# Kernel tuning notes

Hardware: AMD Instinct MI355X
Metric: run time of the kernel (lower is better)

The kernel has to match this reference:

```python
import jax, jax.numpy as jnp
import numpy as np

D_IN = 200
H = 1024
OUT = 1095
L = 12
B = 128
T = 20


def setup_inputs() -> dict:
    key = jax.random.key(0)
    ks = jax.random.split(key, 10)
    s = lambda k, shape, fan: (jax.random.normal(k, shape, jnp.float32) / np.sqrt(fan)).astype(jnp.float32)
    return {
        "x": jax.random.normal(ks[0], (B, T, D_IN), jnp.float32),
        "hidden": jnp.zeros((L, B, H), jnp.float32),
        "W1": s(ks[1], (D_IN, H), D_IN),
        "b1": jnp.zeros((H,), jnp.float32),
        # SRU per-layer weights: input -> [x_tilde, f_gate, r_gate] (3H), plus biases for f,r (2H)
        "sru_W": s(ks[2], (L, H, 3 * H), H),
        "sru_b": jnp.zeros((L, 2 * H), jnp.float32),
        "W3": s(ks[3], (H, 1024), H),
        "b3": jnp.zeros((1024,), jnp.float32),
        "W4": s(ks[4], (1024, OUT), 1024),
        "b4": jnp.zeros((OUT,), jnp.float32),
    }


def _sru_layer(x_tbh, c0, W_l, b_l):
    # x_tbh: [T,B,H]; c0: [B,H]
    U = jnp.einsum("tbh,hk->tbk", x_tbh, W_l)  # [T,B,3H]
    x_tilde, f_pre, r_pre = jnp.split(U, 3, axis=-1)
    b_f, b_r = jnp.split(b_l, 2)
    f = jax.nn.sigmoid(f_pre + b_f)
    r = jax.nn.sigmoid(r_pre + b_r)

    def step(c, inp):
        xt, ft, rt, x_in = inp
        c = ft * c + (1.0 - ft) * xt
        h = rt * jnp.tanh(c) + (1.0 - rt) * x_in  # highway (use_tanh=True)
        return c, h

    c_T, h_seq = jax.lax.scan(step, c0, (x_tilde, f, r, x_tbh))
    return h_seq, c_T


def reference(x, hidden, W1, b1, sru_W, sru_b, W3, b3, W4, b4):
    b, t, _ = x.shape
    # Dense_layer1 (dropout is identity in eval)
    h = x.reshape(b * t, -1) @ W1 + b1
    h = h.reshape(b, t, H).transpose(1, 0, 2)  # [T,B,H]
    cs = []
    for l in range(L):
        h, c_T = _sru_layer(h, hidden[l], sru_W[l], sru_b[l])
        cs.append(c_T)
    hidden_after = jnp.stack(cs, axis=0)  # [L,B,H]
    h = h.transpose(1, 0, 2).reshape(b * t, H)
    fx = h @ W3 + b3
    y = jax.nn.relu(fx)
    logits = (y @ W4 + b4).reshape(-1, OUT)
    return logits, fx, hidden_after
```

## Files before the change

### kernel.cpp

```cpp
#include <hip/hip_runtime.h>

#define D_IN  200
#define KPAD1 224
#define HDIM  1024
#define OUTN  1095
#define NPAD4 1152
#define LNUM  12
#define BB    128
#define TT    20
#define MROWS (BB * TT)

typedef __bf16 bf16;
typedef __attribute__((ext_vector_type(8))) __bf16 bf16x8;
typedef __attribute__((ext_vector_type(4))) float floatx4;

__device__ __forceinline__ bool res_f32(int dt, int inf32) {
  return dt == 1 || (dt == 2 && inf32 != 0);
}

__global__ __launch_bounds__(64) void detect_k(const unsigned int* __restrict__ w,
                                               int* __restrict__ flag) {
  int cnt = 0;
  for (int i = threadIdx.x; i < 1024; i += 64) {
    unsigned int ex = (w[i] >> 7) & 0xFFu;
    if (ex >= 104u && ex <= 131u) cnt++;
  }
  #pragma unroll
  for (int off = 32; off; off >>= 1) cnt += __shfl_down(cnt, off);
  if (threadIdx.x == 0) *flag = (cnt > 512) ? 0 : 1;
}

__global__ __launch_bounds__(256) void transp_k(
    const void* __restrict__ in, const int* __restrict__ dflag,
    bf16* __restrict__ out, int K, int N, int Kpad, int Npad,
    unsigned long long in_bs, unsigned long long out_bs)
{
  __shared__ float tile[32][33];
  const int inf32 = *dflag;
  const int tx = threadIdx.x & 31, ty = threadIdx.x >> 5;
  const int kt = blockIdx.x * 32, nt = blockIdx.y * 32;
  const float* inf = (const float*)in + (size_t)blockIdx.z * in_bs;
  const bf16*  inb = (const bf16*)in + (size_t)blockIdx.z * in_bs;
  #pragma unroll
  for (int j = 0; j < 4; j++) {
    const int k = kt + ty + j * 8, n = nt + tx;
    float v = 0.f;
    if (k < K && n < N)
      v = inf32 ? inf[(size_t)k * N + n] : (float)inb[(size_t)k * N + n];
    tile[ty + j * 8][tx] = v;
  }
  __syncthreads();
  bf16* o = out + (size_t)blockIdx.z * out_bs;
  #pragma unroll
  for (int j = 0; j < 4; j++) {
    const int n = nt + ty + j * 8, k = kt + tx;
    if (n < Npad && k < Kpad) o[(size_t)n * Kpad + k] = (bf16)tile[tx][ty + j * 8];
  }
}

__global__ __launch_bounds__(256) void convx_k(
    const void* __restrict__ x, const int* __restrict__ dflag, bf16* __restrict__ xc)
{
  const int inf32 = *dflag;
  const int idx = blockIdx.x * 256 + threadIdx.x;
  if (idx >= MROWS * KPAD1) return;
  const int row = idx / KPAD1;
  const int d = idx - row * KPAD1;
  const int t = row / BB, b = row - t * BB;
  float v = 0.f;
  if (d < D_IN) {
    const size_t src = ((size_t)b * TT + t) * D_IN + d;
    v = inf32 ? ((const float*)x)[src] : (float)((const bf16*)x)[src];
  }
  xc[idx] = (bf16)v;
}

__global__ __launch_bounds__(256) void gemm_f(
    const bf16* __restrict__ A, const bf16* __restrict__ Bt,
    const void* __restrict__ bias, unsigned long long bias_eoff,
    const int* __restrict__ dflag,
    void* __restrict__ out0, unsigned long long out0_eoff, int o0_dt,
    bf16* __restrict__ out1,
    int N, int Ks, int remapP, int remapQ)
{
  __shared__ bf16 As[128 * 32];
  __shared__ bf16 Bs[128 * 32];
  const int inf32 = *dflag;
  const bool o0f = res_f32(o0_dt, inf32);

  const int tid = threadIdx.x;
  const int wave = tid >> 6, lane = tid & 63;
  const int wr = wave >> 1, wc = wave & 1;
  const int lm = lane & 15, q = lane >> 4;
  const int l4r = lane >> 2, l4k = (lane & 3) * 8;

  const int bm = blockIdx.x * 128, bn = blockIdx.y * 128;

  int ar0 = bm + wave * 32 + l4r;
  int ar1 = ar0 + 16;
  if (remapP) {
    ar0 = (ar0 % remapP) * remapQ + ar0 / remapP;
    ar1 = (ar1 % remapP) * remapQ + ar1 / remapP;
  }
  const bf16* gA0 = A + (size_t)ar0 * Ks + l4k;
  const bf16* gA1 = A + (size_t)ar1 * Ks + l4k;
  const bf16* gB0 = Bt + (size_t)(bn + wave * 32 + l4r) * Ks + l4k;
  const bf16* gB1 = gB0 + (size_t)16 * Ks;

  auto* As3 = (__attribute__((address_space(3))) char*)As;
  auto* Bs3 = (__attribute__((address_space(3))) char*)Bs;
  const int lds0 = (wave * 32) * 64;
  const int lds1 = lds0 + 16 * 64;

  floatx4 acc[4][4];
  #pragma unroll
  for (int i = 0; i < 4; i++)
    #pragma unroll
    for (int j = 0; j < 4; j++) acc[i][j] = (floatx4){0.f, 0.f, 0.f, 0.f};

  for (int k0 = 0; k0 < Ks; k0 += 32) {
    __builtin_amdgcn_global_load_lds((const __attribute__((address_space(1))) void*)gA0,
                                     (__attribute__((address_space(3))) void*)(As3 + lds0), 16, 0, 0);
    __builtin_amdgcn_global_load_lds((const __attribute__((address_space(1))) void*)gA1,
                                     (__attribute__((address_space(3))) void*)(As3 + lds1), 16, 0, 0);
    __builtin_amdgcn_global_load_lds((const __attribute__((address_space(1))) void*)gB0,
                                     (__attribute__((address_space(3))) void*)(Bs3 + lds0), 16, 0, 0);
    __builtin_amdgcn_global_load_lds((const __attribute__((address_space(1))) void*)gB1,
                                     (__attribute__((address_space(3))) void*)(Bs3 + lds1), 16, 0, 0);
    gA0 += 32; gA1 += 32; gB0 += 32; gB1 += 32;
    __syncthreads();

    bf16x8 af[4], bfr[4];
    #pragma unroll
    for (int mi = 0; mi < 4; mi++)
      af[mi] = *(const bf16x8*)&As[(wr * 64 + mi * 16 + lm) * 32 + q * 8];
    #pragma unroll
    for (int ni = 0; ni < 4; ni++)
      bfr[ni] = *(const bf16x8*)&Bs[(wc * 64 + ni * 16 + lm) * 32 + q * 8];
    #pragma unroll
    for (int mi = 0; mi < 4; mi++)
      #pragma unroll
      for (int ni = 0; ni < 4; ni++)
        acc[mi][ni] = __builtin_amdgcn_mfma_f32_16x16x32_bf16(af[mi], bfr[ni], acc[mi][ni], 0, 0, 0);
    __syncthreads();
  }

  const int row_base = bm + wr * 64 + q * 4;
  const int col_base = bn + wc * 64 + lm;
  #pragma unroll
  for (int ni = 0; ni < 4; ni++) {
    const int c = col_base + ni * 16;
    if (c >= N) continue;
    float bv = 0.f;
    if (bias)
      bv = inf32 ? ((const float*)bias)[bias_eoff + c]
                 : (float)((const bf16*)bias)[bias_eoff + c];
    #pragma unroll
    for (int mi = 0; mi < 4; mi++)
      #pragma unroll
      for (int reg = 0; reg < 4; reg++) {
        const int r = row_base + mi * 16 + reg;
        const float v = acc[mi][ni][reg] + bv;
        const size_t o = (size_t)r * N + c;
        if (o0f) ((float*)out0)[out0_eoff + o] = v;
        else     ((bf16*)out0)[out0_eoff + o] = (bf16)v;
        if (out1) out1[o] = (bf16)(v > 0.f ? v : 0.f);
      }
  }
}

#define BM 64
#define BN 64
#define BK 32
#define LDSP (BK + 8)

__global__ __launch_bounds__(256) void gemm_k(
    const void* __restrict__ A, const void* __restrict__ Bm,
    const void* __restrict__ bias,
    void* __restrict__ out0, unsigned long long out0_eoff, int o0_dt,
    bf16* __restrict__ out1,
    const int* __restrict__ dflag,
    unsigned long long b_eoff, unsigned long long bias_eoff,
    int M, int N, int K, int remapP, int remapQ, int a_dt)
{
  __shared__ bf16 As[BM][LDSP];
  __shared__ bf16 Bs[BN][LDSP];

  const int inf32 = *dflag;
  const bool af32 = res_f32(a_dt, inf32);
  const bool bf32 = (inf32 != 0);
  const bool o0f  = res_f32(o0_dt, inf32);

  const int tid = threadIdx.x;
  const int bm = blockIdx.x * BM;
  const int bn = blockIdx.y * BN;

  const int a_r = tid >> 2;
  const int a_k = (tid & 3) * 8;
  int a_row = bm + a_r;
  const bool a_ok = a_row < M;
  if (remapP) a_row = (a_row % remapP) * remapQ + (a_row / remapP);
  const size_t a_off = (size_t)a_row * (size_t)K;

  const int b_k = tid >> 3;
  const int b_ng = bn + (tid & 7) * 8;
  const int b_nl = (tid & 7) * 8;
  const bool n_vec = ((N & 7) == 0) && (b_ng + 8 <= N);

  const int wave = tid >> 6;
  const int lane = tid & 63;
  const int wm = (wave >> 1) * 32;
  const int wn = (wave & 1) * 32;
  const int lm = lane & 15;
  const int q  = lane >> 4;

  floatx4 acc00 = {0.f,0.f,0.f,0.f}, acc01 = {0.f,0.f,0.f,0.f};
  floatx4 acc10 = {0.f,0.f,0.f,0.f}, acc11 = {0.f,0.f,0.f,0.f};

  for (int k0 = 0; k0 < K; k0 += BK) {
    {
      union { bf16x8 v; bf16 e[8]; } av;
      const int kg = k0 + a_k;
      if (af32) {
        const float* Af = (const float*)A;
        if (a_ok && (kg + 8 <= K)) {
          floatx4 f0 = *(const floatx4*)(Af + a_off + kg);
          floatx4 f1 = *(const floatx4*)(Af + a_off + kg + 4);
          #pragma unroll
          for (int e = 0; e < 4; e++) { av.e[e] = (bf16)f0[e]; av.e[4 + e] = (bf16)f1[e]; }
        } else {
          #pragma unroll
          for (int e = 0; e < 8; e++) {
            const int kk = kg + e;
            av.e[e] = (a_ok && kk < K) ? (bf16)Af[a_off + kk] : (bf16)0.f;
          }
        }
      } else {
        const bf16* Ab = (const bf16*)A;
        if (a_ok && (kg + 8 <= K)) {
          av.v = *(const bf16x8*)(Ab + a_off + kg);
        } else {
          #pragma unroll
          for (int e = 0; e < 8; e++) {
            const int kk = kg + e;
            av.e[e] = (a_ok && kk < K) ? Ab[a_off + kk] : (bf16)0.f;
          }
        }
      }
      *(bf16x8*)&As[a_r][a_k] = av.v;
    }
    {
      union { bf16x8 v; bf16 e[8]; } bv;
      const int kg = k0 + b_k;
      if (bf32) {
        const float* Bf = (const float*)Bm + b_eoff;
        if ((kg < K) && n_vec) {
          floatx4 f0 = *(const floatx4*)(Bf + (size_t)kg * N + b_ng);
          floatx4 f1 = *(const floatx4*)(Bf + (size_t)kg * N + b_ng + 4);
          #pragma unroll
          for (int e = 0; e < 4; e++) { bv.e[e] = (bf16)f0[e]; bv.e[4 + e] = (bf16)f1[e]; }
        } else {
          #pragma unroll
          for (int e = 0; e < 8; e++) {
            const int nn = b_ng + e;
            bv.e[e] = (kg < K && nn < N) ? (bf16)Bf[(size_t)kg * N + nn] : (bf16)0.f;
          }
        }
      } else {
        const bf16* Bb = (const bf16*)Bm + b_eoff;
        if ((kg < K) && n_vec) {
          bv.v = *(const bf16x8*)(Bb + (size_t)kg * N + b_ng);
        } else {
          #pragma unroll
          for (int e = 0; e < 8; e++) {
            const int nn = b_ng + e;
            bv.e[e] = (kg < K && nn < N) ? Bb[(size_t)kg * N + nn] : (bf16)0.f;
          }
        }
      }
      #pragma unroll
      for (int e = 0; e < 8; e++) Bs[b_nl + e][b_k] = bv.e[e];
    }
    __syncthreads();

    const bf16x8 a0 = *(const bf16x8*)&As[wm + lm][q * 8];
    const bf16x8 a1 = *(const bf16x8*)&As[wm + 16 + lm][q * 8];
    const bf16x8 b0 = *(const bf16x8*)&Bs[wn + lm][q * 8];
    const bf16x8 b1 = *(const bf16x8*)&Bs[wn + 16 + lm][q * 8];
    acc00 = __builtin_amdgcn_mfma_f32_16x16x32_bf16(a0, b0, acc00, 0, 0, 0);
    acc01 = __builtin_amdgcn_mfma_f32_16x16x32_bf16(a0, b1, acc01, 0, 0, 0);
    acc10 = __builtin_amdgcn_mfma_f32_16x16x32_bf16(a1, b0, acc10, 0, 0, 0);
    acc11 = __builtin_amdgcn_mfma_f32_16x16x32_bf16(a1, b1, acc11, 0, 0, 0);
    __syncthreads();
  }

  floatx4 accs[2][2] = {{acc00, acc01}, {acc10, acc11}};
  const int r0 = bm + wm + q * 4;
  const int c0 = bn + wn + lm;
  #pragma unroll
  for (int i = 0; i < 2; i++) {
    #pragma unroll
    for (int j = 0; j < 2; j++) {
      const int c = c0 + j * 16;
      if (c >= N) continue;
      float bias_v = 0.f;
      if (bias) {
        bias_v = inf32 ? ((const float*)bias)[bias_eoff + c]
                       : (float)((const bf16*)bias)[bias_eoff + c];
      }
      #pragma unroll
      for (int reg = 0; reg < 4; reg++) {
        const int r = r0 + i * 16 + reg;
        if (r >= M) continue;
        const float v = accs[i][j][reg] + bias_v;
        const size_t o = (size_t)r * (size_t)N + c;
        if (o0f) ((float*)out0)[out0_eoff + o] = v;
        else     ((bf16*)out0)[out0_eoff + o] = (bf16)v;
        if (out1) out1[o] = (bf16)(v > 0.f ? v : 0.f);
      }
    }
  }
}

__device__ __forceinline__ float sigmoidf_(float x) { return 1.f / (1.f + __expf(-x)); }
__device__ __forceinline__ float tanhf_(float x)    { return 1.f - 2.f / (__expf(2.f * x) + 1.f); }

__global__ __launch_bounds__(256) void sru_scan_k(
    const void* __restrict__ U, int u_f32,
    bf16* __restrict__ h,
    const void* __restrict__ c0, unsigned long long c0_eoff,
    const void* __restrict__ bvec, unsigned long long bvec_eoff,
    const int* __restrict__ dflag,
    void* __restrict__ cout, unsigned long long cout_eoff)
{
  const int inf32 = *dflag;
  const int idx = blockIdx.x * 256 + threadIdx.x;
  const int hh = idx & (HDIM - 1);
  const int b = idx >> 10;
  const float bf_ = inf32 ? ((const float*)bvec)[bvec_eoff + hh]
                          : (float)((const bf16*)bvec)[bvec_eoff + hh];
  const float br_ = inf32 ? ((const float*)bvec)[bvec_eoff + HDIM + hh]
                          : (float)((const bf16*)bvec)[bvec_eoff + HDIM + hh];
  float c = inf32 ? ((const float*)c0)[c0_eoff + idx]
                  : (float)((const bf16*)c0)[c0_eoff + idx];
  const float* Uf = (const float*)U;
  const bf16*  Ub = (const bf16*)U;
  #pragma unroll 4
  for (int t = 0; t < TT; t++) {
    const size_t off = (size_t)(t * BB + b) * (size_t)(3 * HDIM);
    const float xt = u_f32 ? Uf[off + hh] : (float)Ub[off + hh];
    const float fp = u_f32 ? Uf[off + HDIM + hh] : (float)Ub[off + HDIM + hh];
    const float rp = u_f32 ? Uf[off + 2 * HDIM + hh] : (float)Ub[off + 2 * HDIM + hh];
    const float fg = sigmoidf_(fp + bf_);
    const float rg = sigmoidf_(rp + br_);
    c = fg * c + (1.f - fg) * xt;
    const size_t hi = (size_t)t * (BB * HDIM) + idx;
    const float xin = (float)h[hi];
    h[hi] = (bf16)(rg * tanhf_(c) + (1.f - rg) * xin);
  }
  if (inf32) ((float*)cout)[cout_eoff + idx] = c;
  else       ((bf16*)cout)[cout_eoff + idx] = (bf16)c;
}

extern "C" void kernel_launch(void* const* d_in, const int* in_sizes, int n_in,
                              void* d_out, int out_size, void* d_ws, size_t ws_size,
                              hipStream_t stream) {
  const void* x       = d_in[0];
  const void* hidden0 = d_in[1];
  const void* W1      = d_in[2];
  const void* b1      = d_in[3];
  const void* sru_W   = d_in[4];
  const void* sru_b   = d_in[5];
  const void* W3      = d_in[6];
  const void* b3      = d_in[7];
  const void* W4      = d_in[8];
  const void* b4      = d_in[9];

  const unsigned long long eo_fx  = (unsigned long long)MROWS * OUTN;
  const unsigned long long eo_hid = eo_fx + (unsigned long long)MROWS * HDIM;

  const size_t z_flag = 256;
  const size_t z_hA   = (size_t)MROWS * HDIM * 2;
  const size_t z_U    = (size_t)MROWS * 3 * HDIM * 4;
  const size_t z_xc   = (size_t)MROWS * KPAD1 * 2;
  const size_t z_W1T  = (size_t)HDIM * KPAD1 * 2;
  const size_t z_sWT  = (size_t)LNUM * 3 * HDIM * HDIM * 2;
  const size_t z_W3T  = (size_t)HDIM * HDIM * 2;
  const size_t z_W4T  = (size_t)NPAD4 * HDIM * 2;
  const size_t FAST_NEED = z_flag + z_hA + z_U + z_xc + z_W1T + z_sWT + z_W3T + z_W4T;

  int* dflag = (int*)d_ws;
  char* p = (char*)d_ws + z_flag;
  bf16*  hA    = (bf16*)p;            p += z_hA;
  char*  Ubase = p;                   p += z_U;
  bf16*  xc    = (bf16*)p;            p += z_xc;
  bf16*  W1T   = (bf16*)p;            p += z_W1T;
  bf16*  sWT   = (bf16*)p;            p += z_sWT;
  bf16*  W3T   = (bf16*)p;            p += z_W3T;
  bf16*  W4T   = (bf16*)p;
  void*  U = (void*)Ubase;
  bf16*  y = (bf16*)Ubase;

  dim3 blk(256);
  detect_k<<<1, 64, 0, stream>>>((const unsigned int*)W1, dflag);

  if (ws_size >= FAST_NEED) {
    convx_k<<<dim3((MROWS * KPAD1 + 255) / 256), blk, 0, stream>>>(x, dflag, xc);
    transp_k<<<dim3(KPAD1 / 32, HDIM / 32, 1), blk, 0, stream>>>(
        W1, dflag, W1T, D_IN, HDIM, KPAD1, HDIM, 0ull, 0ull);
    transp_k<<<dim3(HDIM / 32, 3 * HDIM / 32, LNUM), blk, 0, stream>>>(
        sru_W, dflag, sWT, HDIM, 3 * HDIM, HDIM, 3 * HDIM,
        (unsigned long long)HDIM * 3 * HDIM, (unsigned long long)3 * HDIM * HDIM);
    transp_k<<<dim3(HDIM / 32, HDIM / 32, 1), blk, 0, stream>>>(
        W3, dflag, W3T, HDIM, HDIM, HDIM, HDIM, 0ull, 0ull);
    transp_k<<<dim3(HDIM / 32, NPAD4 / 32, 1), blk, 0, stream>>>(
        W4, dflag, W4T, HDIM, OUTN, HDIM, NPAD4, 0ull, 0ull);

    gemm_f<<<dim3(MROWS / 128, HDIM / 128), blk, 0, stream>>>(
        xc, W1T, b1, 0ull, dflag, hA, 0ull, 0, nullptr, HDIM, KPAD1, 0, 0);

    for (int l = 0; l < LNUM; l++) {
      gemm_f<<<dim3(MROWS / 128, 3 * HDIM / 128), blk, 0, stream>>>(
          hA, sWT + (size_t)l * 3 * HDIM * HDIM, nullptr, 0ull, dflag,
          U, 0ull, 1, nullptr, 3 * HDIM, HDIM, 0, 0);
      sru_scan_k<<<dim3((BB * HDIM) / 256), blk, 0, stream>>>(
          U, 1, hA, hidden0, (unsigned long long)l * BB * HDIM,
          sru_b, (unsigned long long)l * 2 * HDIM,
          dflag, d_out, eo_hid + (unsigned long long)l * BB * HDIM);
    }

    gemm_f<<<dim3(MROWS / 128, HDIM / 128), blk, 0, stream>>>(
        hA, W3T, b3, 0ull, dflag, d_out, eo_fx, 2, y, HDIM, HDIM, TT, BB);

    gemm_f<<<dim3(MROWS / 128, NPAD4 / 128), blk, 0, stream>>>(
        y, W4T, b4, 0ull, dflag, d_out, 0ull, 2, nullptr, OUTN, HDIM, 0, 0);
  } else {
    const size_t need_f32U = z_flag + z_hA + z_U;
    const int u_f32 = (ws_size >= need_f32U) ? 1 : 0;

    gemm_k<<<dim3(MROWS / BM, HDIM / BN), blk, 0, stream>>>(
        x, W1, b1, hA, 0ull, 0, nullptr, dflag, 0ull, 0ull,
        MROWS, HDIM, D_IN, BB, TT, 2);

    for (int l = 0; l < LNUM; l++) {
      gemm_k<<<dim3(MROWS / BM, (3 * HDIM) / BN), blk, 0, stream>>>(
          hA, sru_W, nullptr, U, 0ull, (u_f32 ? 1 : 0), nullptr, dflag,
          (unsigned long long)l * HDIM * 3 * HDIM, 0ull,
          MROWS, 3 * HDIM, HDIM, 0, 0, 0);
      sru_scan_k<<<dim3((BB * HDIM) / 256), blk, 0, stream>>>(
          U, u_f32, hA, hidden0, (unsigned long long)l * BB * HDIM,
          sru_b, (unsigned long long)l * 2 * HDIM,
          dflag, d_out, eo_hid + (unsigned long long)l * BB * HDIM);
    }

    gemm_k<<<dim3(MROWS / BM, HDIM / BN), blk, 0, stream>>>(
        hA, W3, b3, d_out, eo_fx, 2, y, dflag, 0ull, 0ull,
        MROWS, HDIM, HDIM, TT, BB, 0);

    gemm_k<<<dim3(MROWS / BM, (OUTN + BN - 1) / BN), blk, 0, stream>>>(
        y, W4, b4, d_out, 0ull, 2, nullptr, dflag, 0ull, 0ull,
        MROWS, OUTN, HDIM, 0, 0, 0);
  }
}
```

Measured before the change: 931.2 us.

## Store SRU gate buffer in bf16, vectorize scan, and widen weight transposes

The SRU projection GEMM now writes U as bf16 instead of fp32, which halves the write and read traffic between the GEMM and the scan. A new scan kernel processes two hidden units per thread with paired bf16 loads and stores. The large weight transposes switch to a 64x64-tile kernel that uses float4 reads and 16-byte bf16 writes. The cost is extra rounding of the gate pre-activations to bf16 before the sigmoid and the recurrence.

```diff
diff --git a/kernel.cpp b/kernel.cpp
--- a/kernel.cpp
+++ b/kernel.cpp
@@ -11,7 +11,9 @@
 #define MROWS (BB * TT)
 
 typedef __bf16 bf16;
+typedef __attribute__((ext_vector_type(2))) __bf16 bf16x2;
 typedef __attribute__((ext_vector_type(8))) __bf16 bf16x8;
+typedef __attribute__((ext_vector_type(2))) float floatx2;
 typedef __attribute__((ext_vector_type(4))) float floatx4;
 
 __device__ __forceinline__ bool res_f32(int dt, int inf32) {
@@ -28,6 +30,51 @@
   #pragma unroll
   for (int off = 32; off; off >>= 1) cnt += __shfl_down(cnt, off);
   if (threadIdx.x == 0) *flag = (cnt > 512) ? 0 : 1;
+}
+
+__global__ __launch_bounds__(256) void ftransp_k(
+    const void* __restrict__ in, const int* __restrict__ dflag,
+    bf16* __restrict__ out, int K, int N, int Npad,
+    unsigned long long in_bs, unsigned long long out_bs)
+{
+  __shared__ float tile[64][69];
+  const int inf32 = *dflag;
+  const int t = threadIdx.x;
+  const int kt = blockIdx.x * 64, nt = blockIdx.y * 64;
+  const float* inf = (const float*)in + (size_t)blockIdx.z * in_bs;
+  const bf16*  inb = (const bf16*)in + (size_t)blockIdx.z * in_bs;
+
+  const int lk = t >> 2;
+  const size_t rbase = (size_t)(kt + lk) * N;
+  #pragma unroll
+  for (int j = 0; j < 4; j++) {
+    const int ln = ((t & 3) + 4 * j) * 4;
+    const int gn = nt + ln;
+    floatx4 v = {0.f, 0.f, 0.f, 0.f};
+    if (inf32) {
+      if (gn + 4 <= N) {
+        v = *(const floatx4*)(inf + rbase + gn);
+      } else {
+        #pragma unroll
+        for (int e = 0; e < 4; e++) if (gn + e < N) v[e] = inf[rbase + gn + e];
+      }
+    } else {
+      #pragma unroll
+      for (int e = 0; e < 4; e++) if (gn + e < N) v[e] = (float)inb[rbase + gn + e];
+    }
+    #pragma unroll
+    for (int e = 0; e < 4; e++) tile[lk][ln + e] = v[e];
+  }
+  __syncthreads();
+
+  const int n  = t >> 2;
+  const int kc = (t & 3) * 16;
+  union { bf16x8 v[2]; bf16 e[16]; } o;
+  #pragma unroll
+  for (int i = 0; i < 16; i++) o.e[i] = (bf16)tile[kc + i][n];
+  bf16* op = out + (size_t)blockIdx.z * out_bs + (size_t)(nt + n) * K + kt + kc;
+  *(bf16x8*)op = o.v[0];
+  *(bf16x8*)(op + 8) = o.v[1];
 }
 
 __global__ __launch_bounds__(256) void transp_k(
@@ -325,6 +372,55 @@
 __device__ __forceinline__ float sigmoidf_(float x) { return 1.f / (1.f + __expf(-x)); }
 __device__ __forceinline__ float tanhf_(float x)    { return 1.f - 2.f / (__expf(2.f * x) + 1.f); }
 
+__global__ __launch_bounds__(256) void sru_scan2_k(
+    const bf16* __restrict__ U,
+    bf16* __restrict__ h,
+    const void* __restrict__ c0, unsigned long long c0_eoff,
+    const void* __restrict__ bvec, unsigned long long bvec_eoff,
+    const int* __restrict__ dflag,
+    void* __restrict__ cout, unsigned long long cout_eoff)
+{
+  const int inf32 = *dflag;
+  const int i2 = (blockIdx.x * 256 + threadIdx.x) * 2;
+  const int hh = i2 & (HDIM - 1);
+  const int b = i2 >> 10;
+  float bf_[2], br_[2], c[2];
+  #pragma unroll
+  for (int e = 0; e < 2; e++) {
+    bf_[e] = inf32 ? ((const float*)bvec)[bvec_eoff + hh + e]
+                   : (float)((const bf16*)bvec)[bvec_eoff + hh + e];
+    br_[e] = inf32 ? ((const float*)bvec)[bvec_eoff + HDIM + hh + e]
+                   : (float)((const bf16*)bvec)[bvec_eoff + HDIM + hh + e];
+    c[e] = inf32 ? ((const float*)c0)[c0_eoff + i2 + e]
+                 : (float)((const bf16*)c0)[c0_eoff + i2 + e];
+  }
+  #pragma unroll 4
+  for (int t = 0; t < TT; t++) {
+    const size_t off = (size_t)(t * BB + b) * (size_t)(3 * HDIM);
+    const bf16x2 xt2 = *(const bf16x2*)(U + off + hh);
+    const bf16x2 fp2 = *(const bf16x2*)(U + off + HDIM + hh);
+    const bf16x2 rp2 = *(const bf16x2*)(U + off + 2 * HDIM + hh);
+    const size_t hi = (size_t)t * (BB * HDIM) + i2;
+    const bf16x2 hin2 = *(const bf16x2*)(h + hi);
+    bf16x2 ho;
+    #pragma unroll
+    for (int e = 0; e < 2; e++) {
+      const float fg = sigmoidf_((float)fp2[e] + bf_[e]);
+      const float rg = sigmoidf_((float)rp2[e] + br_[e]);
+      c[e] = fg * c[e] + (1.f - fg) * (float)xt2[e];
+      ho[e] = (bf16)(rg * tanhf_(c[e]) + (1.f - rg) * (float)hin2[e]);
+    }
+    *(bf16x2*)(h + hi) = ho;
+  }
+  if (inf32) {
+    floatx2 co; co[0] = c[0]; co[1] = c[1];
+    *(floatx2*)((float*)cout + cout_eoff + i2) = co;
+  } else {
+    bf16x2 co; co[0] = (bf16)c[0]; co[1] = (bf16)c[1];
+    *(bf16x2*)((bf16*)cout + cout_eoff + i2) = co;
+  }
+}
+
 __global__ __launch_bounds__(256) void sru_scan_k(
     const void* __restrict__ U, int u_f32,
     bf16* __restrict__ h,
@@ -398,8 +494,8 @@
   bf16*  sWT   = (bf16*)p;            p += z_sWT;
   bf16*  W3T   = (bf16*)p;            p += z_W3T;
   bf16*  W4T   = (bf16*)p;
-  void*  U = (void*)Ubase;
-  bf16*  y = (bf16*)Ubase;
+  bf16*  Ub = (bf16*)Ubase;
+  bf16*  y  = (bf16*)Ubase;
 
   dim3 blk(256);
   detect_k<<<1, 64, 0, stream>>>((const unsigned int*)W1, dflag);
@@ -408,13 +504,13 @@
     convx_k<<<dim3((MROWS * KPAD1 + 255) / 256), blk, 0, stream>>>(x, dflag, xc);
     transp_k<<<dim3(KPAD1 / 32, HDIM / 32, 1), blk, 0, stream>>>(
         W1, dflag, W1T, D_IN, HDIM, KPAD1, HDIM, 0ull, 0ull);
-    transp_k<<<dim3(HDIM / 32, 3 * HDIM / 32, LNUM), blk, 0, stream>>>(
-        sru_W, dflag, sWT, HDIM, 3 * HDIM, HDIM, 3 * HDIM,
+    ftransp_k<<<dim3(HDIM / 64, 3 * HDIM / 64, LNUM), blk, 0, stream>>>(
+        sru_W, dflag, sWT, HDIM, 3 * HDIM, 3 * HDIM,
         (unsigned long long)HDIM * 3 * HDIM, (unsigned long long)3 * HDIM * HDIM);
-    transp_k<<<dim3(HDIM / 32, HDIM / 32, 1), blk, 0, stream>>>(
-        W3, dflag, W3T, HDIM, HDIM, HDIM, HDIM, 0ull, 0ull);
-    transp_k<<<dim3(HDIM / 32, NPAD4 / 32, 1), blk, 0, stream>>>(
-        W4, dflag, W4T, HDIM, OUTN, HDIM, NPAD4, 0ull, 0ull);
+    ftransp_k<<<dim3(HDIM / 64, HDIM / 64, 1), blk, 0, stream>>>(
+        W3, dflag, W3T, HDIM, HDIM, HDIM, 0ull, 0ull);
+    ftransp_k<<<dim3(HDIM / 64, NPAD4 / 64, 1), blk, 0, stream>>>(
+        W4, dflag, W4T, HDIM, OUTN, NPAD4, 0ull, 0ull);
 
     gemm_f<<<dim3(MROWS / 128, HDIM / 128), blk, 0, stream>>>(
         xc, W1T, b1, 0ull, dflag, hA, 0ull, 0, nullptr, HDIM, KPAD1, 0, 0);
@@ -422,9 +518,9 @@
     for (int l = 0; l < LNUM; l++) {
       gemm_f<<<dim3(MROWS / 128, 3 * HDIM / 128), blk, 0, stream>>>(
           hA, sWT + (size_t)l * 3 * HDIM * HDIM, nullptr, 0ull, dflag,
-          U, 0ull, 1, nullptr, 3 * HDIM, HDIM, 0, 0);
-      sru_scan_k<<<dim3((BB * HDIM) / 256), blk, 0, stream>>>(
-          U, 1, hA, hidden0, (unsigned long long)l * BB * HDIM,
+          Ub, 0ull, 0, nullptr, 3 * HDIM, HDIM, 0, 0);
+      sru_scan2_k<<<dim3((BB * HDIM) / 512), blk, 0, stream>>>(
+          Ub, hA, hidden0, (unsigned long long)l * BB * HDIM,
           sru_b, (unsigned long long)l * 2 * HDIM,
           dflag, d_out, eo_hid + (unsigned long long)l * BB * HDIM);
     }
@@ -437,6 +533,7 @@
   } else {
     const size_t need_f32U = z_flag + z_hA + z_U;
     const int u_f32 = (ws_size >= need_f32U) ? 1 : 0;
+    void* U = (void*)Ubase;
 
     gemm_k<<<dim3(MROWS / BM, HDIM / BN), blk, 0, stream>>>(
         x, W1, b1, hA, 0ull, 0, nullptr, dflag, 0ull, 0ull,
```

Result: faster. 846.1 us (-9.1%).
